# Kernel optimization log

Measured on AMD Instinct MI355X. Metric: run time of the kernel, lower is better.

## Reference

```python
import jax, jax.numpy as jnp
import numpy as np

NUM_NODES = 324
IN_DIM, HID_DIM, OUT_DIM = 128, 256, 64
BN_EPS = 1e-5
HUB_COLS = [7, 9, 24, 45, 59, 62, 63, 66, 67, 69, 70, 73, 74, 76, 77, 80, 81, 84,
            95, 97, 99, 114, 116, 118, 143, 147, 150, 152, 156, 158, 159, 163, 167, 171]


def _adj_norm() -> jnp.ndarray:
    """D^{-1/2} A D^{-1/2} for the fixed 324-node template graph (edge weights = 1)."""
    adj = np.eye(NUM_NODES, dtype=np.float32)
    cols = np.array(HUB_COLS)
    for r in range(300, NUM_NODES):
        adj[r, cols] = 1.0
        adj[cols, r] = 1.0
    deg = adj.sum(axis=1)
    dinv = 1.0 / np.sqrt(deg)
    return jnp.asarray(adj * dinv[:, None] * dinv[None, :])


def setup_inputs() -> dict:
    key = jax.random.key(0)
    ks = jax.random.split(key, 6)
    batch = 1024
    x = jax.random.normal(ks[0], (batch, NUM_NODES, IN_DIM), dtype=jnp.float32)
    # Xavier-uniform linear weights (PyG GCNConv lin has weight [out, in]), zero bias
    lim1 = float(np.sqrt(6.0 / (IN_DIM + HID_DIM)))
    W1 = jax.random.uniform(ks[1], (HID_DIM, IN_DIM), jnp.float32, -lim1, lim1)
    b1 = jnp.zeros((HID_DIM,), jnp.float32)
    lim2 = float(np.sqrt(6.0 / (HID_DIM + OUT_DIM)))
    W2 = jax.random.uniform(ks[2], (OUT_DIM, HID_DIM), jnp.float32, -lim2, lim2)
    b2 = jnp.zeros((OUT_DIM,), jnp.float32)
    # BatchNorm1d(hidden_dim) params + running stats (inference mode)
    gamma = jax.random.uniform(ks[3], (HID_DIM,), jnp.float32, 0.5, 1.5)
    beta = 0.1 * jax.random.normal(ks[4], (HID_DIM,), jnp.float32)
    running_mean = jnp.zeros((HID_DIM,), jnp.float32)
    running_var = jnp.ones((HID_DIM,), jnp.float32)
    return {"x": x, "W1": W1, "b1": b1, "W2": W2, "b2": b2,
            "gamma": gamma, "beta": beta,
            "running_mean": running_mean, "running_var": running_var,
            "adj_norm": _adj_norm()}


def reference(x, W1, b1, W2, b2, gamma, beta, running_mean, running_var, adj_norm):
    # Layer 0: GCNConv = aggregate(norm_adj, x @ W^T) + b  (batched over b)
    h = jnp.einsum("bnf,hf->bnh", x, W1)               # lin
    h = jnp.einsum("nm,bmh->bnh", adj_norm, h) + b1    # normalized scatter-aggregate
    h = jnp.where(h >= 0, h, 0.01 * h)                 # leaky_relu(0.01)
    # dropout: identity at inference
    h = (h - running_mean) * gamma * jax.lax.rsqrt(running_var + BN_EPS) + beta
    # Layer 1 (final): GCNConv only
    out = jnp.einsum("bnh,oh->bno", h, W2)
    out = jnp.einsum("nm,bmo->bno", adj_norm, out) + b2
    return out
```

## Files before the change

kernel.cpp:

```cpp
#include <hip/hip_runtime.h>

#define NN   324
#define INF  128
#define HID  256
#define OUTF 64

#define DINV_R 0.16903085f
#define DINV_H 0.2f

#define W1B_OFF 655360
#define W2B_OFF 671744
#define BNP_OFF 679936

typedef float  f32x16 __attribute__((ext_vector_type(16)));
typedef short  short8 __attribute__((ext_vector_type(8)));

__constant__ int HUBC[34] = {7, 9, 24, 45, 59, 62, 63, 66, 67, 69, 70, 73, 74, 76,
                             77, 80, 81, 84, 95, 97, 99, 114, 116, 118, 143, 147,
                             150, 152, 156, 158, 159, 163, 167, 171};

#define HW0 ((1ULL<<7)|(1ULL<<9)|(1ULL<<24)|(1ULL<<45)|(1ULL<<59)|(1ULL<<62)|(1ULL<<63))
#define HW1 ((1ULL<<2)|(1ULL<<3)|(1ULL<<5)|(1ULL<<6)|(1ULL<<9)|(1ULL<<10)|(1ULL<<12)|(1ULL<<13)| \
             (1ULL<<16)|(1ULL<<17)|(1ULL<<20)|(1ULL<<31)|(1ULL<<33)|(1ULL<<35)|(1ULL<<50)|(1ULL<<52)|(1ULL<<54))
#define HW2 ((1ULL<<15)|(1ULL<<19)|(1ULL<<22)|(1ULL<<24)|(1ULL<<28)|(1ULL<<30)|(1ULL<<31)| \
             (1ULL<<35)|(1ULL<<39)|(1ULL<<43))

__device__ __forceinline__ bool is_hub(int n) {
    if (n >= 192) return false;
    unsigned long long w = (n < 64) ? HW0 : (n < 128 ? HW1 : HW2);
    return (w >> (n & 63)) & 1ULL;
}
__device__ __forceinline__ unsigned int f2bf1(float f) {
    unsigned int u = __builtin_bit_cast(unsigned int, f);
    return (u + 0x7fffu + ((u >> 16) & 1u)) >> 16;
}
__device__ __forceinline__ float bf2f(unsigned short h) {
    return __builtin_bit_cast(float, (unsigned int)h << 16);
}
__device__ __forceinline__ unsigned int f2bf2(float lo, float hi) {
    return f2bf1(lo) | (f2bf1(hi) << 16);
}
__device__ __forceinline__ uint4 pack8(float4 a, float4 b) {
    uint4 r;
    r.x = f2bf2(a.x, a.y); r.y = f2bf2(a.z, a.w);
    r.z = f2bf2(b.x, b.y); r.w = f2bf2(b.z, b.w);
    return r;
}
__device__ __forceinline__ short8 as_s8(uint4 u) {
    union { uint4 u; short8 s; } t; t.u = u; return t.s;
}

__global__ __launch_bounds__(256) void gcn_k00(
    const float* __restrict__ W1, const float* __restrict__ W2,
    const float* __restrict__ b1, const float* __restrict__ gamma,
    const float* __restrict__ beta, const float* __restrict__ rmean,
    const float* __restrict__ rvar, float* __restrict__ ws)
{
    const int blk = blockIdx.x, tid = threadIdx.x;
    if (blk < 16) {
        int p = blk * 256 + tid;
        int l31 = p & 31, hi = (p >> 5) & 1, ks = (p >> 6) & 7, htc = p >> 9;
        int h = htc * 32 + l31;
        int k0 = ks * 16 + hi * 8;
        const float4* s = (const float4*)(W1 + (size_t)h * INF + k0);
        ((uint4*)(ws + W1B_OFF))[p] = pack8(s[0], s[1]);
    } else if (blk < 24) {
        int p = (blk - 16) * 256 + tid;
        int l31 = p & 31, hi = (p >> 5) & 1, ot = (p >> 6) & 1, ks2 = (p >> 7) & 1, kc = p >> 8;
        int o = ot * 32 + l31;
        int k0 = kc * 32 + ks2 * 16 + hi * 8;
        const float4* s = (const float4*)(W2 + (size_t)o * HID + k0);
        ((uint4*)(ws + W2B_OFF))[p] = pack8(s[0], s[1]);
    } else {
        float sc = gamma[tid] * rsqrtf(rvar[tid] + 1e-5f);
        ((float4*)(ws + BNP_OFF))[tid] =
            make_float4(b1[tid], sc, beta[tid] - rmean[tid] * sc, 0.f);
    }
}

__global__ __launch_bounds__(256, 3) void gcn_k0(
    const float* __restrict__ x,  const float* __restrict__ b1,
    const float* __restrict__ W2, const float* __restrict__ gamma,
    const float* __restrict__ beta, const float* __restrict__ rmean,
    const float* __restrict__ rvar, float* __restrict__ ws)
{
    __shared__ uint4 Xs[16 * 67];
    __shared__ float sv1[2][256];
    __shared__ float vpart[2][2][256];
    __shared__ float vHl[2][256];

    const int tid = threadIdx.x, lane = tid & 63, w = tid >> 6;
    const int mt = w >> 1, nh = w & 1, l31 = lane & 31, hi = lane >> 5;
    const int b = blockIdx.x;
    const float* xb = x + (size_t)b * NN * INF;
    float* wsb = ws + (size_t)b * 640;
    const uint4* W1B2q = (const uint4*)(ws + W1B_OFF);

    for (int p = tid; p < 64 * 16; p += 256) {
        int lr = p >> 4, kg = p & 15;
        uint4 v = {0u, 0u, 0u, 0u};
        if (lr < 58) {
            int gr = (lr < 24) ? 300 + lr : HUBC[lr - 24];
            const float4* s = (const float4*)(xb + (size_t)gr * INF + kg * 8);
            v = pack8(s[0], s[1]);
        }
        Xs[kg * 67 + lr] = v;
    }
    __syncthreads();

    if (tid < 128) {
        int kg = tid >> 3, sub = tid & 7;
        const unsigned short* xs = (const unsigned short*)Xs;
        float s1 = 0.f, s2 = 0.f;
        for (int lr = 0; lr < 24; ++lr)  s1 += bf2f(xs[(kg * 67 + lr) * 8 + sub]);
        for (int lr = 24; lr < 58; ++lr) s2 += bf2f(xs[(kg * 67 + lr) * 8 + sub]);
        unsigned short* xw = (unsigned short*)Xs;
        xw[(kg * 67 + 58) * 8 + sub] = (unsigned short)f2bf1(s1 * DINV_R);
        xw[(kg * 67 + 59) * 8 + sub] = (unsigned short)f2bf1(s2 * DINV_H);
    }
    __syncthreads();

    f32x16 acc[4];
#pragma unroll
    for (int i = 0; i < 4; ++i)
#pragma unroll
        for (int j = 0; j < 16; ++j) acc[i][j] = 0.f;

#pragma unroll
    for (int ks = 0; ks < 8; ++ks) {
        short8 af = as_s8(Xs[(2 * ks + hi) * 67 + mt * 32 + l31]);
#pragma unroll
        for (int ntl = 0; ntl < 4; ++ntl) {
            short8 bf = as_s8(W1B2q[((nh * 4 + ntl) * 8 + ks) * 64 + lane]);
            acc[ntl] = __builtin_amdgcn_mfma_f32_32x32x16_bf16(af, bf, acc[ntl], 0, 0, 0);
        }
    }

    if (mt == 1 && hi == 0) {
#pragma unroll
        for (int ntl = 0; ntl < 4; ++ntl) {
            int col = nh * 128 + ntl * 32 + l31;
            float r58 = acc[ntl][14], r59 = acc[ntl][15];
            sv1[0][col] = r58;  sv1[1][col] = r59;
            wsb[col] = r58;     wsb[256 + col] = r59;
        }
    }
    __syncthreads();

    float p1[4] = {0.f, 0.f, 0.f, 0.f}, p2[4] = {0.f, 0.f, 0.f, 0.f};
#pragma unroll
    for (int ntl = 0; ntl < 4; ++ntl) {
        int col = nh * 128 + ntl * 32 + l31;
        float bias  = b1[col];
        float scale = gamma[col] * rsqrtf(rvar[col] + 1e-5f);
        float off   = beta[col] - rmean[col] * scale;
        float svA = sv1[0][col], svB = sv1[1][col];
#pragma unroll
        for (int q = 0; q < 16; ++q) {
            int lr = mt * 32 + (q & 3) + 8 * (q >> 2) + 4 * hi;
            bool isR = lr < 24, isH = (lr >= 24 && lr < 58);
            float d   = isR ? DINV_R : (isH ? DINV_H : 0.f);
            float oth = isR ? svB : svA;
            float v = d * d * acc[ntl][q] + d * oth + bias;
            v = fmaxf(v, 0.01f * v);
            float z = v * scale + off;
            p1[ntl] += isR ? DINV_R * z : 0.f;
            p2[ntl] += isH ? DINV_H * z : 0.f;
        }
    }
#pragma unroll
    for (int ntl = 0; ntl < 4; ++ntl) {
        p1[ntl] += __shfl_xor(p1[ntl], 32);
        p2[ntl] += __shfl_xor(p2[ntl], 32);
    }
    if (hi == 0) {
#pragma unroll
        for (int ntl = 0; ntl < 4; ++ntl) {
            int col = nh * 128 + ntl * 32 + l31;
            vpart[mt][0][col] = p1[ntl];
            vpart[mt][1][col] = p2[ntl];
        }
    }
    __syncthreads();
    for (int i = tid; i < 512; i += 256) {
        int which = i >> 8, col = i & 255;
        vHl[which][col] = vpart[0][which][col] + vpart[1][which][col];
    }
    __syncthreads();

    if (tid < 128) {
        int vr = tid >> 6, oc = tid & 63;
        const float* w2r = W2 + (size_t)oc * HID;
        float s = 0.f;
        for (int k = 0; k < 256; k += 8) {
#pragma unroll
            for (int i = 0; i < 8; ++i) s += vHl[vr][k + i] * w2r[k + i];
        }
        wsb[512 + vr * 64 + oc] = s;
    }
}

#define XSTR 65
#define HSTR 66
__global__ __launch_bounds__(256, 6) void gcn_k1(
    const float* __restrict__ x, const float* __restrict__ b2,
    const float* __restrict__ ws, float* __restrict__ out)
{
    __shared__ uint4  Xs[16 * XSTR];
    __shared__ uint4  Hs[8 * HSTR];
    __shared__ float4 tab[64];

    const int tid = threadIdx.x, lane = tid & 63, w = tid >> 6;
    const int mt = w >> 1, nc = w & 1, l31 = lane & 31, hi = lane >> 5;
    const int bid = blockIdx.x;
    const int b = bid / 6, m6 = bid - b * 6;
    const float* xb  = x + ((size_t)b * NN + m6 * 64) * INF;
    const float* wsb = ws + (size_t)b * 640;
    const uint4*  W1B2q = (const uint4*)(ws + W1B_OFF);
    const uint4*  W2B2q = (const uint4*)(ws + W2B_OFF);
    const float4* bnp   = (const float4*)(ws + BNP_OFF);

    if (tid < 64) {
        int gr = m6 * 64 + tid;
        float4 t;
        if (gr >= NN)          t = make_float4(0.f, 0.f, 0.f, 0.f);
        else if (gr >= 300)    t = make_float4(DINV_R * DINV_R, 0.f, DINV_R, 0.f);
        else if (is_hub(gr))   t = make_float4(DINV_H * DINV_H, DINV_H, 0.f, 0.f);
        else                   t = make_float4(1.f, 0.f, 0.f, 0.f);
        tab[tid] = t;
    }
    for (int p = tid; p < 64 * 16; p += 256) {
        int n = p >> 4, kg = p & 15;
        uint4 v = {0u, 0u, 0u, 0u};
        if (m6 * 64 + n < NN) {
            const float4* s = (const float4*)(xb + n * INF + kg * 8);
            v = pack8(s[0], s[1]);
        }
        Xs[kg * XSTR + n] = v;
    }
    __syncthreads();

    f32x16 acc2;
#pragma unroll
    for (int j = 0; j < 16; ++j) acc2[j] = 0.f;

    const int cl = nc * 32 + l31;

    for (int hc = 0; hc < 4; ++hc) {
        const int gcol = hc * 64 + cl;
        f32x16 acc1;
#pragma unroll
        for (int j = 0; j < 16; ++j) acc1[j] = 0.f;
        const uint4* w1q = W1B2q + (size_t)(hc * 2 + nc) * 512 + lane;
#pragma unroll
        for (int ks = 0; ks < 8; ++ks) {
            short8 bf = as_s8(w1q[ks * 64]);
            short8 af = as_s8(Xs[(2 * ks + hi) * XSTR + mt * 32 + l31]);
            acc1 = __builtin_amdgcn_mfma_f32_32x32x16_bf16(af, bf, acc1, 0, 0, 0);
        }
        const float4 bn = bnp[gcol];
        const float Sv = wsb[gcol], Tv = wsb[256 + gcol];

        __syncthreads();
        {
            unsigned short* hw = (unsigned short*)Hs;
            const int kg2 = cl >> 3, sub = cl & 7;
#pragma unroll
            for (int q = 0; q < 16; ++q) {
                int n = mt * 32 + (q & 3) + 8 * (q >> 2) + 4 * hi;
                float4 t = tab[n];
                float v = t.x * acc1[q] + t.y * Sv + t.z * Tv + bn.x;
                v = fmaxf(v, 0.01f * v);
                float z = v * bn.y + bn.z;
                hw[(kg2 * HSTR + n) * 8 + sub] = (unsigned short)f2bf1(z);
            }
        }
        __syncthreads();

        const uint4* w2q = W2B2q + (size_t)hc * 512 + nc * 64 + lane;
#pragma unroll
        for (int ks = 0; ks < 4; ++ks) {
            short8 bf = as_s8(w2q[ks * 128]);
            short8 af = as_s8(Hs[(2 * ks + hi) * HSTR + mt * 32 + l31]);
            acc2 = __builtin_amdgcn_mfma_f32_32x32x16_bf16(af, bf, acc2, 0, 0, 0);
        }
    }

    {
        float* Ol = (float*)Xs;
        const float Sv2 = wsb[512 + cl], Tv2 = wsb[576 + cl], bias2 = b2[cl];
#pragma unroll
        for (int q = 0; q < 16; ++q) {
            int n = mt * 32 + (q & 3) + 8 * (q >> 2) + 4 * hi;
            float4 t = tab[n];
            Ol[n * 64 + cl] = t.x * acc2[q] + t.y * Sv2 + t.z * Tv2 + bias2;
        }
    }
    __syncthreads();

    {
        const float* Ol = (const float*)Xs;
        float* ob = out + ((size_t)b * NN + m6 * 64) * OUTF;
#pragma unroll
        for (int i = 0; i < 4; ++i) {
            int p = tid + i * 256;
            int n = p >> 4, c4 = p & 15;
            if (m6 * 64 + n < NN)
                *(float4*)(ob + n * 64 + c4 * 4) = *(const float4*)(Ol + n * 64 + c4 * 4);
        }
    }
}

extern "C" void kernel_launch(void* const* d_in, const int* in_sizes, int n_in,
                              void* d_out, int out_size, void* d_ws, size_t ws_size,
                              hipStream_t stream) {
    const float* x     = (const float*)d_in[0];
    const float* W1    = (const float*)d_in[1];
    const float* b1    = (const float*)d_in[2];
    const float* W2    = (const float*)d_in[3];
    const float* b2    = (const float*)d_in[4];
    const float* gamma = (const float*)d_in[5];
    const float* beta  = (const float*)d_in[6];
    const float* rmean = (const float*)d_in[7];
    const float* rvar  = (const float*)d_in[8];
    float* out = (float*)d_out;
    float* ws  = (float*)d_ws;

    gcn_k00<<<dim3(25), dim3(256), 0, stream>>>(W1, W2, b1, gamma, beta,
                                                rmean, rvar, ws);
    gcn_k0<<<dim3(1024), dim3(256), 0, stream>>>(x, b1, W2, gamma, beta,
                                                 rmean, rvar, ws);
    gcn_k1<<<dim3(6144), dim3(256), 0, stream>>>(x, b2, ws, out);
}
```

Baseline: 168.0 us.

## Give each wave its own 32-row tile with private LDS and no block barriers

```diff
diff --git a/kernel.cpp b/kernel.cpp
--- a/kernel.cpp
+++ b/kernel.cpp
@@ -200,113 +200,121 @@
     }
 }
 
-#define XSTR 65
-#define HSTR 66
-__global__ __launch_bounds__(256, 6) void gcn_k1(
+#define PSTR 33
+#define LDS_XW   0
+#define LDS_HW   33792
+#define LDS_TW   50688
+#define LDS_K1   52736
+__global__ __launch_bounds__(256, 3) void gcn_k1(
     const float* __restrict__ x, const float* __restrict__ b2,
     const float* __restrict__ ws, float* __restrict__ out)
 {
-    __shared__ uint4  Xs[16 * XSTR];
-    __shared__ uint4  Hs[8 * HSTR];
-    __shared__ float4 tab[64];
-
+    extern __shared__ char smem[];
     const int tid = threadIdx.x, lane = tid & 63, w = tid >> 6;
-    const int mt = w >> 1, nc = w & 1, l31 = lane & 31, hi = lane >> 5;
+    const int l31 = lane & 31, hi = lane >> 5;
+    uint4*  Xw = (uint4*)(smem + LDS_XW) + w * (16 * PSTR);
+    uint4*  Hw = (uint4*)(smem + LDS_HW) + w * (8 * PSTR);
+    float4* tw = (float4*)(smem + LDS_TW) + w * 32;
+
     const int bid = blockIdx.x;
-    const int b = bid / 6, m6 = bid - b * 6;
-    const float* xb  = x + ((size_t)b * NN + m6 * 64) * INF;
+    const int b = bid / 3, m3 = bid - b * 3;
+    const int row0 = m3 * 128 + w * 32;
+    const float* xb  = x + ((size_t)b * NN + row0) * INF;
     const float* wsb = ws + (size_t)b * 640;
-    const uint4*  W1B2q = (const uint4*)(ws + W1B_OFF);
-    const uint4*  W2B2q = (const uint4*)(ws + W2B_OFF);
-    const float4* bnp   = (const float4*)(ws + BNP_OFF);
-
-    if (tid < 64) {
-        int gr = m6 * 64 + tid;
+    const uint4*  W1q = (const uint4*)(ws + W1B_OFF);
+    const uint4*  W2q = (const uint4*)(ws + W2B_OFF);
+    const float4* bnp = (const float4*)(ws + BNP_OFF);
+
+    if (hi == 0) {
+        int gr = row0 + l31;
         float4 t;
-        if (gr >= NN)          t = make_float4(0.f, 0.f, 0.f, 0.f);
-        else if (gr >= 300)    t = make_float4(DINV_R * DINV_R, 0.f, DINV_R, 0.f);
-        else if (is_hub(gr))   t = make_float4(DINV_H * DINV_H, DINV_H, 0.f, 0.f);
-        else                   t = make_float4(1.f, 0.f, 0.f, 0.f);
-        tab[tid] = t;
-    }
-    for (int p = tid; p < 64 * 16; p += 256) {
+        if (gr >= NN)        t = make_float4(0.f, 0.f, 0.f, 0.f);
+        else if (gr >= 300)  t = make_float4(DINV_R * DINV_R, 0.f, DINV_R, 0.f);
+        else if (is_hub(gr)) t = make_float4(DINV_H * DINV_H, DINV_H, 0.f, 0.f);
+        else                 t = make_float4(1.f, 0.f, 0.f, 0.f);
+        tw[l31] = t;
+    }
+#pragma unroll
+    for (int i = 0; i < 8; ++i) {
+        int p = lane + i * 64;
         int n = p >> 4, kg = p & 15;
         uint4 v = {0u, 0u, 0u, 0u};
-        if (m6 * 64 + n < NN) {
-            const float4* s = (const float4*)(xb + n * INF + kg * 8);
+        if (row0 + n < NN) {
+            const float4* s = (const float4*)(xb + (size_t)n * INF + kg * 8);
             v = pack8(s[0], s[1]);
         }
-        Xs[kg * XSTR + n] = v;
-    }
-    __syncthreads();
-
-    f32x16 acc2;
-#pragma unroll
-    for (int j = 0; j < 16; ++j) acc2[j] = 0.f;
-
-    const int cl = nc * 32 + l31;
-
+        Xw[kg * PSTR + n] = v;
+    }
+
+    const float sv2a = wsb[512 + l31],      tv2a = wsb[576 + l31],      bba = b2[l31];
+    const float sv2b = wsb[512 + 32 + l31], tv2b = wsb[576 + 32 + l31], bbb = b2[32 + l31];
+
+    f32x16 acc2a, acc2b;
+#pragma unroll
+    for (int j = 0; j < 16; ++j) { acc2a[j] = 0.f; acc2b[j] = 0.f; }
+
+#pragma unroll
     for (int hc = 0; hc < 4; ++hc) {
-        const int gcol = hc * 64 + cl;
-        f32x16 acc1;
-#pragma unroll
-        for (int j = 0; j < 16; ++j) acc1[j] = 0.f;
-        const uint4* w1q = W1B2q + (size_t)(hc * 2 + nc) * 512 + lane;
-#pragma unroll
-        for (int ks = 0; ks < 8; ++ks) {
-            short8 bf = as_s8(w1q[ks * 64]);
-            short8 af = as_s8(Xs[(2 * ks + hi) * XSTR + mt * 32 + l31]);
-            acc1 = __builtin_amdgcn_mfma_f32_32x32x16_bf16(af, bf, acc1, 0, 0, 0);
-        }
-        const float4 bn = bnp[gcol];
-        const float Sv = wsb[gcol], Tv = wsb[256 + gcol];
-
-        __syncthreads();
-        {
-            unsigned short* hw = (unsigned short*)Hs;
-            const int kg2 = cl >> 3, sub = cl & 7;
+        f32x16 acc1[2];
+#pragma unroll
+        for (int j = 0; j < 2; ++j)
+#pragma unroll
+            for (int q = 0; q < 16; ++q) acc1[j][q] = 0.f;
+#pragma unroll
+        for (int j = 0; j < 2; ++j) {
+            const uint4* w1 = W1q + (size_t)((hc * 2 + j) * 8) * 64 + lane;
+#pragma unroll
+            for (int ks = 0; ks < 8; ++ks) {
+                short8 aX = as_s8(Xw[(2 * ks + hi) * PSTR + l31]);
+                acc1[j] = __builtin_amdgcn_mfma_f32_32x32x16_bf16(
+                              aX, as_s8(w1[ks * 64]), acc1[j], 0, 0, 0);
+            }
+        }
+#pragma unroll
+        for (int j = 0; j < 2; ++j) {
+            const int h = hc * 64 + j * 32 + l31;
+            const float4 bn = bnp[h];
+            const float Sv = wsb[h], Tv = wsb[256 + h];
+            unsigned short* hw = (unsigned short*)Hw;
+            const int kg = j * 4 + (l31 >> 3), sub = l31 & 7;
 #pragma unroll
             for (int q = 0; q < 16; ++q) {
-                int n = mt * 32 + (q & 3) + 8 * (q >> 2) + 4 * hi;
-                float4 t = tab[n];
-                float v = t.x * acc1[q] + t.y * Sv + t.z * Tv + bn.x;
+                int n = (q & 3) + 8 * (q >> 2) + 4 * hi;
+                float4 t = tw[n];
+                float v = t.x * acc1[j][q] + t.y * Sv + t.z * Tv + bn.x;
                 v = fmaxf(v, 0.01f * v);
                 float z = v * bn.y + bn.z;
-                hw[(kg2 * HSTR + n) * 8 + sub] = (unsigned short)f2bf1(z);
+                hw[(kg * PSTR + n) * 8 + sub] = (unsigned short)f2bf1(z);
             }
         }
-        __syncthreads();
-
-        const uint4* w2q = W2B2q + (size_t)hc * 512 + nc * 64 + lane;
 #pragma unroll
         for (int ks = 0; ks < 4; ++ks) {
-            short8 bf = as_s8(w2q[ks * 128]);
-            short8 af = as_s8(Hs[(2 * ks + hi) * HSTR + mt * 32 + l31]);
-            acc2 = __builtin_amdgcn_mfma_f32_32x32x16_bf16(af, bf, acc2, 0, 0, 0);
+            short8 aH = as_s8(Hw[(2 * ks + hi) * PSTR + l31]);
+            short8 b0 = as_s8(W2q[(size_t)(((hc * 4 + ks) * 2 + 0)) * 64 + lane]);
+            short8 b1f = as_s8(W2q[(size_t)(((hc * 4 + ks) * 2 + 1)) * 64 + lane]);
+            acc2a = __builtin_amdgcn_mfma_f32_32x32x16_bf16(aH, b0, acc2a, 0, 0, 0);
+            acc2b = __builtin_amdgcn_mfma_f32_32x32x16_bf16(aH, b1f, acc2b, 0, 0, 0);
         }
     }
 
     {
-        float* Ol = (float*)Xs;
-        const float Sv2 = wsb[512 + cl], Tv2 = wsb[576 + cl], bias2 = b2[cl];
+        float* Ol = (float*)Xw;
 #pragma unroll
         for (int q = 0; q < 16; ++q) {
-            int n = mt * 32 + (q & 3) + 8 * (q >> 2) + 4 * hi;
-            float4 t = tab[n];
-            Ol[n * 64 + cl] = t.x * acc2[q] + t.y * Sv2 + t.z * Tv2 + bias2;
-        }
-    }
-    __syncthreads();
-
-    {
-        const float* Ol = (const float*)Xs;
-        float* ob = out + ((size_t)b * NN + m6 * 64) * OUTF;
-#pragma unroll
-        for (int i = 0; i < 4; ++i) {
-            int p = tid + i * 256;
+            int n = (q & 3) + 8 * (q >> 2) + 4 * hi;
+            float4 t = tw[n];
+            Ol[n * 64 + l31]      = t.x * acc2a[q] + t.y * sv2a + t.z * tv2a + bba;
+            Ol[n * 64 + 32 + l31] = t.x * acc2b[q] + t.y * sv2b + t.z * tv2b + bbb;
+        }
+        const float* Olr = (const float*)Xw;
+        float* ob = out + ((size_t)b * NN + row0) * OUTF;
+#pragma unroll
+        for (int i = 0; i < 8; ++i) {
+            int p = lane + i * 64;
             int n = p >> 4, c4 = p & 15;
-            if (m6 * 64 + n < NN)
-                *(float4*)(ob + n * 64 + c4 * 4) = *(const float4*)(Ol + n * 64 + c4 * 4);
+            if (row0 + n < NN)
+                *(float4*)(ob + (size_t)n * OUTF + c4 * 4) =
+                    *(const float4*)(Olr + n * 64 + c4 * 4);
         }
     }
 }
@@ -330,5 +338,7 @@
                                                 rmean, rvar, ws);
     gcn_k0<<<dim3(1024), dim3(256), 0, stream>>>(x, b1, W2, gamma, beta,
                                                  rmean, rvar, ws);
-    gcn_k1<<<dim3(6144), dim3(256), 0, stream>>>(x, b2, ws, out);
-}
+    hipFuncSetAttribute((const void*)gcn_k1,
+                        hipFuncAttributeMaxDynamicSharedMemorySize, LDS_K1);
+    gcn_k1<<<dim3(3072), dim3(256), LDS_K1, stream>>>(x, b2, ws, out);
+}
```

After: 187.0 us. +11.3%, slower.
